# Kernel optimization log

Measured on AMD Instinct MI355X. Metric: run time of the kernel, lower is better.

The kernel has to match this reference:

```python
import jax, jax.numpy as jnp
import numpy as np
import math

N_HEADS = 16
D_MODEL = 1024
HEAD_DIM = D_MODEL // N_HEADS
ROPE_THETA = 10000.0


def _rope_cos_sin(seq_len, head_dim, dtype):
    # freqs = 1/theta^(2i/d), angles = outer(t, freqs)  -> [seq_len, head_dim//2]
    inv_freq = 1.0 / (ROPE_THETA ** (jnp.arange(0, head_dim, 2, dtype=jnp.float32) / head_dim))
    ang = jnp.arange(seq_len, dtype=jnp.float32)[:, None] * inv_freq[None, :]
    return jnp.cos(ang).astype(dtype), jnp.sin(ang).astype(dtype)


def _apply_rope(t, cos, sin):
    # t: [B, N, H, D]; treat last dim as complex pairs (a, b); multiply by e^{i*ang}
    B, N, H, D = t.shape
    tr = t.reshape(B, N, H, D // 2, 2)
    a, b = tr[..., 0], tr[..., 1]
    c = cos[None, :, None, :]  # [1, N, 1, D/2]
    s = sin[None, :, None, :]
    out = jnp.stack([a * c - b * s, a * s + b * c], axis=-1)
    return out.reshape(B, N, H, D)


def setup_inputs() -> dict:
    key = jax.random.key(0)
    ks = jax.random.split(key, 9)
    B, N, D = 4, 2048, D_MODEL
    scale = 0.02
    inp = {"x": jax.random.normal(ks[0], (B, N, D), dtype=jnp.float32)}
    for i, nm in enumerate(["q", "k", "v", "o"]):
        inp[f"w{nm}"] = jax.random.normal(ks[1 + 2 * i], (D, D), dtype=jnp.float32) * scale
        inp[f"b{nm}"] = jax.random.normal(ks[2 + 2 * i], (D,), dtype=jnp.float32) * scale
    return inp


def reference(x, wq, bq, wk, bk, wv, bv, wo, bo):
    B, N, D = x.shape
    H, Hd = N_HEADS, HEAD_DIM
    q = (x @ wq.T + bq).reshape(B, N, H, Hd)
    k = (x @ wk.T + bk).reshape(B, N, H, Hd)
    v = (x @ wv.T + bv).reshape(B, N, H, Hd)
    cos, sin = _rope_cos_sin(N, Hd, x.dtype)
    q = _apply_rope(q, cos, sin)
    k = _apply_rope(k, cos, sin)
    # SDPA, no mask, eval mode (dropout_p = 0)
    scores = jnp.einsum("bqhd,bkhd->bhqk", q, k) / math.sqrt(Hd)
    attn = jax.nn.softmax(scores, axis=-1)
    out = jnp.einsum("bhqk,bkhd->bqhd", attn, v)  # [B, N, H, Hd]
    out = out.reshape(B, N, D)
    return out @ wo.T + bo
```

## Files before the change

### kernel.cpp

```cpp
#include <hip/hip_runtime.h>
#include <math.h>
#include <stdint.h>

#define BBATCH 4
#define NTOK   2048
#define DMOD   1024
#define NH     16
#define HD     64
#define MTOT   8192

typedef __bf16 bf16;
typedef __bf16 bf16x4 __attribute__((ext_vector_type(4)));
typedef __bf16 bf16x8 __attribute__((ext_vector_type(8)));
typedef float  f32x4  __attribute__((ext_vector_type(4)));

typedef __attribute__((address_space(3))) unsigned int lds_u32;
typedef __attribute__((address_space(1))) unsigned int glb_u32;

__device__ __forceinline__ void gload16(const bf16* g, bf16* l) {
    __builtin_amdgcn_global_load_lds((glb_u32*)g, (lds_u32*)l, 16, 0, 0);
}

#define QSCALE 0.1803368801111204f

__global__ void rope_table_kernel(float* __restrict__ ct, float* __restrict__ st) {
    int idx = blockIdx.x * 256 + threadIdx.x;
    if (idx >= NTOK * 32) return;
    int n = idx >> 5, p = idx & 31;
    float inv = powf(10000.0f, -(float)(2 * p) / 64.0f);
    float ang = (float)n * inv;
    ct[idx] = cosf(ang);
    st[idx] = sinf(ang);
}

__global__ __launch_bounds__(256)
void convert_kernel(const float* __restrict__ x,  const float* __restrict__ wq,
                    const float* __restrict__ wk, const float* __restrict__ wv,
                    const float* __restrict__ wo,
                    bf16* __restrict__ xb,  bf16* __restrict__ wqb,
                    bf16* __restrict__ wkb, bf16* __restrict__ wvb,
                    bf16* __restrict__ wob)
{
    const int X4 = (MTOT * DMOD) / 4;
    const int W4 = (DMOD * DMOD) / 4;
    int i = blockIdx.x * 256 + threadIdx.x;
    const float* src; bf16* dst; int off;
    if (i < X4) { src = x; dst = xb; off = i; }
    else {
        int j = i - X4; int w = j / W4; off = j - w * W4;
        src = (w == 0) ? wq : (w == 1) ? wk : (w == 2) ? wv : wo;
        dst = (w == 0) ? wqb : (w == 1) ? wkb : (w == 2) ? wvb : wob;
    }
    float4 v = ((const float4*)src)[off];
    bf16x4 o;
    o[0] = (bf16)v.x; o[1] = (bf16)v.y; o[2] = (bf16)v.z; o[3] = (bf16)v.w;
    *(bf16x4*)(dst + (size_t)off * 4) = o;
}


#define GEMM_PROLOGUE(Aptr, Wptr)                                              \
    __shared__ __align__(16) bf16 As[2][128 * 32];                             \
    __shared__ __align__(16) bf16 Bs[2][128 * 32];                             \
    const int tid = threadIdx.x;                                               \
    const int l   = tid & 63;                                                  \
    const int wid = tid >> 6;                                                  \
    const int wm  = wid >> 1, wn = wid & 1;                                    \
    const int fr  = l & 15, fg = l >> 4;                                       \
    const int srow  = tid >> 2;                                                \
    const int sslot = (tid & 3) ^ ((srow >> 1) & 3);                           \
    const bf16* gA0 = (Aptr) + (size_t)(m0 + srow) * 1024 + sslot * 8;         \
    const bf16* gB0 = (Wptr) + (size_t)(n0 + srow) * 1024 + sslot * 8;         \
    const int aswz = (fg ^ ((fr >> 1) & 3)) * 8;                               \
    int aoff[4], boff[4];                                                      \
    _Pragma("unroll")                                                          \
    for (int i = 0; i < 4; ++i) {                                              \
        aoff[i] = (wm * 64 + i * 16 + fr) * 32 + aswz;                         \
        boff[i] = (wn * 64 + i * 16 + fr) * 32 + aswz;                         \
    }                                                                          \
    f32x4 acc[4][4] = {};

#define GSTAGE(kt, b) do {                                         \
        const bf16* a0_ = gA0 + (kt) * 32;                         \
        const bf16* b0_ = gB0 + (kt) * 32;                         \
        gload16(a0_,                      As[b] + tid * 8);        \
        gload16(a0_ + (size_t)64 * 1024,  As[b] + 2048 + tid * 8); \
        gload16(b0_,                      Bs[b] + tid * 8);        \
        gload16(b0_ + (size_t)64 * 1024,  Bs[b] + 2048 + tid * 8); \
    } while (0)

#define GEMM_KLOOP                                                             \
    GSTAGE(0, 0);                                                              \
    __syncthreads();                                                           \
    int cur = 0;                                                               \
    for (int kt = 0; kt < 32; ++kt) {                                          \
        if (kt < 31) GSTAGE(kt + 1, cur ^ 1);                                  \
        bf16x8 af[4], bfv[4];                                                  \
        _Pragma("unroll")                                                      \
        for (int i = 0; i < 4; ++i) af[i]  = *(const bf16x8*)(As[cur] + aoff[i]); \
        _Pragma("unroll")                                                      \
        for (int i = 0; i < 4; ++i) bfv[i] = *(const bf16x8*)(Bs[cur] + boff[i]); \
        _Pragma("unroll")                                                      \
        for (int mi = 0; mi < 4; ++mi)                                         \
            _Pragma("unroll")                                                  \
            for (int ni = 0; ni < 4; ++ni)                                     \
                acc[mi][ni] = __builtin_amdgcn_mfma_f32_16x16x32_bf16(         \
                    af[mi], bfv[ni], acc[mi][ni], 0, 0, 0);                    \
        __syncthreads();                                                       \
        cur ^= 1;                                                              \
    }

__global__ __launch_bounds__(256)
void gemm_qkv(const bf16* __restrict__ A,
              const bf16* __restrict__ wq, const bf16* __restrict__ wk,
              const bf16* __restrict__ wv,
              const float* __restrict__ bq, const float* __restrict__ bk,
              const float* __restrict__ bv,
              bf16* __restrict__ qb, bf16* __restrict__ kb, bf16* __restrict__ vtb,
              const float* __restrict__ ct, const float* __restrict__ st)
{
    const int sel = blockIdx.x >> 3;
    const int n0  = (blockIdx.x & 7) * 128;
    const int m0  = blockIdx.y * 128;
    const bf16*  W    = (sel == 0) ? wq : (sel == 1) ? wk : wv;
    const float* bias = (sel == 0) ? bq : (sel == 1) ? bk : bv;
    bf16*        out  = (sel == 0) ? qb : (sel == 1) ? kb : vtb;

    GEMM_PROLOGUE(A, W)
    GEMM_KLOOP

    if (sel == 2) {
#pragma unroll
        for (int ni = 0; ni < 4; ++ni) {
            const int col = n0 + wn * 64 + ni * 16 + fr;
            const int h = col >> 6, dd = col & 63;
            const float bvv = bias[col];
#pragma unroll
            for (int mi = 0; mi < 4; ++mi) {
                const int rowb = m0 + wm * 64 + mi * 16 + fg * 4;
                const int bi = rowb >> 11, npb = rowb & (NTOK - 1);
                bf16x4 ov;
#pragma unroll
                for (int r = 0; r < 4; ++r) ov[r] = (bf16)(acc[mi][ni][r] + bvv);
                *(bf16x4*)(out + ((size_t)(bi * NH + h) * HD + dd) * NTOK + npb) = ov;
            }
        }
    } else {
        const float scale = (sel == 0) ? QSCALE : 1.0f;
#pragma unroll
        for (int ni = 0; ni < 4; ++ni) {
            const int col = n0 + wn * 64 + ni * 16 + fr;
            const int h = col >> 6, dd = col & 63, p = (dd >> 1);
            const float bvv = bias[col];
#pragma unroll
            for (int mi = 0; mi < 4; ++mi) {
                const int rowb = m0 + wm * 64 + mi * 16 + fg * 4;
#pragma unroll
                for (int r = 0; r < 4; ++r) {
                    const int row = rowb + r;
                    const int bi = row >> 11, np = row & (NTOK - 1);
                    float v  = acc[mi][ni][r] + bvv;
                    float pv = __shfl_xor(v, 1);
                    float c = ct[np * 32 + p], s = st[np * 32 + p];
                    float o = (dd & 1) ? (pv * s + v * c) : (v * c - pv * s);
                    o *= scale;
                    out[((size_t)(bi * NH + h) * NTOK + np) * HD + dd] = (bf16)o;
                }
            }
        }
    }
}

__global__ __launch_bounds__(256)
void gemm_oproj(const bf16* __restrict__ A, const bf16* __restrict__ W,
                const float* __restrict__ bias, float* __restrict__ out)
{
    const int m0 = blockIdx.y * 128, n0 = blockIdx.x * 128;
    GEMM_PROLOGUE(A, W)
    GEMM_KLOOP
#pragma unroll
    for (int ni = 0; ni < 4; ++ni) {
        const int col = n0 + wn * 64 + ni * 16 + fr;
        const float bv = bias[col];
#pragma unroll
        for (int mi = 0; mi < 4; ++mi) {
            const int rowb = m0 + wm * 64 + mi * 16 + fg * 4;
#pragma unroll
            for (int r = 0; r < 4; ++r)
                out[(size_t)(rowb + r) * 1024 + col] = acc[mi][ni][r] + bv;
        }
    }
}

__global__ __launch_bounds__(256)
void attn_mfma(const bf16* __restrict__ Q, const bf16* __restrict__ K,
               const bf16* __restrict__ Vt, bf16* __restrict__ out)
{
    __shared__ __align__(16) bf16 Ks[2][64 * 64];
    __shared__ __align__(16) bf16 Vs[2][64 * 64];
    __shared__ __align__(16) bf16 Ps[4][32 * 64];

    const int tid = threadIdx.x;
    const int l   = tid & 63;
    const int wid = tid >> 6;
    const int fr  = l & 15, fg = l >> 4;
    const int q0 = blockIdx.x * 128;
    const int bh = blockIdx.y;

    const bf16* Qb = Q  + (size_t)bh * NTOK * HD;
    const bf16* Kb = K  + (size_t)bh * NTOK * HD;
    const bf16* Vb = Vt + (size_t)bh * HD * NTOK;
    bf16* Pw = Ps[wid];

    bf16x8 qf[2][2];
#pragma unroll
    for (int nq = 0; nq < 2; ++nq)
#pragma unroll
        for (int ks = 0; ks < 2; ++ks)
            qf[nq][ks] = *(const bf16x8*)(Qb + (size_t)(q0 + wid * 32 + nq * 16 + fr) * HD
                                          + ks * 32 + fg * 8);

    bf16x8 ones;
#pragma unroll
    for (int i = 0; i < 8; ++i) ones[i] = (bf16)1.0f;

    const int srow  = tid >> 3;
    const int sslot = (tid & 7) ^ (srow & 7);
    const bf16* gK0 = Kb + (size_t)srow * HD + sslot * 8;
    const bf16* gV0 = Vb + (size_t)srow * NTOK + sslot * 8;

#define ASTAGE(t, b) do {                                          \
        const bf16* gK_ = gK0 + (size_t)(t) * 64 * HD;             \
        const bf16* gV_ = gV0 + (size_t)(t) * 64;                  \
        gload16(gK_,                      Ks[b] + tid * 8);        \
        gload16(gK_ + 32 * HD,            Ks[b] + 2048 + tid * 8); \
        gload16(gV_,                      Vs[b] + tid * 8);        \
        gload16(gV_ + (size_t)32 * NTOK,  Vs[b] + 2048 + tid * 8); \
    } while (0)

    f32x4 o[4][2] = {};
    f32x4 l4[2] = {};

    ASTAGE(0, 0);
    __syncthreads();
    int cur = 0;

    for (int t = 0; t < 32; ++t) {
        if (t < 31) ASTAGE(t + 1, cur ^ 1);
        const bf16* Kc = Ks[cur];
        const bf16* Vc = Vs[cur];

        f32x4 tt[4][2] = {};
#pragma unroll
        for (int ks = 0; ks < 2; ++ks) {
            bf16x8 kf[4];
#pragma unroll
            for (int mk = 0; mk < 4; ++mk)
                kf[mk] = *(const bf16x8*)(Kc + (mk * 16 + fr) * 64
                                          + (((ks * 4 + fg) ^ (fr & 7)) * 8));
#pragma unroll
            for (int mk = 0; mk < 4; ++mk)
#pragma unroll
                for (int nq = 0; nq < 2; ++nq)
                    tt[mk][nq] = __builtin_amdgcn_mfma_f32_16x16x32_bf16(
                        kf[mk], qf[nq][ks], tt[mk][nq], 0, 0, 0);
        }

#pragma unroll
        for (int nq = 0; nq < 2; ++nq) {
#pragma unroll
            for (int mk = 0; mk < 4; ++mk) {
                bf16x4 pk;
#pragma unroll
                for (int r = 0; r < 4; ++r)
                    pk[r] = (bf16)__builtin_amdgcn_exp2f(tt[mk][nq][r]);
                *(bf16x4*)(Pw + (nq * 16 + fr) * 64
                           + (((2 * mk + (fg >> 1)) ^ (fr & 7)) * 8) + (fg & 1) * 4) = pk;
            }
        }

#pragma unroll
        for (int ks = 0; ks < 2; ++ks) {
            bf16x8 vf[4], pf[2];
#pragma unroll
            for (int md = 0; md < 4; ++md)
                vf[md] = *(const bf16x8*)(Vc + (md * 16 + fr) * 64
                                          + (((ks * 4 + fg) ^ (fr & 7)) * 8));
#pragma unroll
            for (int nq = 0; nq < 2; ++nq)
                pf[nq] = *(const bf16x8*)(Pw + (nq * 16 + fr) * 64
                                          + (((ks * 4 + fg) ^ (fr & 7)) * 8));
#pragma unroll
            for (int md = 0; md < 4; ++md)
#pragma unroll
                for (int nq = 0; nq < 2; ++nq)
                    o[md][nq] = __builtin_amdgcn_mfma_f32_16x16x32_bf16(
                        vf[md], pf[nq], o[md][nq], 0, 0, 0);
#pragma unroll
            for (int nq = 0; nq < 2; ++nq)
                l4[nq] = __builtin_amdgcn_mfma_f32_16x16x32_bf16(
                    ones, pf[nq], l4[nq], 0, 0, 0);
        }

        __syncthreads();
        cur ^= 1;
    }
#undef ASTAGE

    const int b_ = bh >> 4, h = bh & 15;
#pragma unroll
    for (int nq = 0; nq < 2; ++nq) {
        const float inv = 1.0f / l4[nq][0];
        const int token = q0 + wid * 32 + nq * 16 + fr;
#pragma unroll
        for (int md = 0; md < 4; ++md) {
            bf16x4 ov;
#pragma unroll
            for (int r = 0; r < 4; ++r) ov[r] = (bf16)(o[md][nq][r] * inv);
            *(bf16x4*)(out + (size_t)(b_ * NTOK + token) * DMOD + h * HD + md * 16 + fg * 4) = ov;
        }
    }
}

extern "C" void kernel_launch(void* const* d_in, const int* in_sizes, int n_in,
                              void* d_out, int out_size, void* d_ws, size_t ws_size,
                              hipStream_t stream)
{
    (void)in_sizes; (void)n_in; (void)out_size; (void)ws_size;

    const float* x  = (const float*)d_in[0];
    const float* wq = (const float*)d_in[1];
    const float* bq = (const float*)d_in[2];
    const float* wk = (const float*)d_in[3];
    const float* bk = (const float*)d_in[4];
    const float* wv = (const float*)d_in[5];
    const float* bv = (const float*)d_in[6];
    const float* wo = (const float*)d_in[7];
    const float* bo = (const float*)d_in[8];
    float* out = (float*)d_out;

    const size_t XSZ = (size_t)MTOT * DMOD;
    const size_t WSZ = (size_t)DMOD * DMOD;
    bf16* xb  = (bf16*)d_ws;
    bf16* wqb = xb  + XSZ;
    bf16* wkb = wqb + WSZ;
    bf16* wvb = wkb + WSZ;
    bf16* wob = wvb + WSZ;
    bf16* qb  = wob + WSZ;
    bf16* kb  = qb  + XSZ;
    bf16* vtb = kb  + XSZ;
    bf16* ab  = vtb + XSZ;
    float* ct = (float*)(ab + XSZ);
    float* st = ct + (size_t)NTOK * 32;

    rope_table_kernel<<<dim3(256), dim3(256), 0, stream>>>(ct, st);
    convert_kernel<<<dim3(12288), dim3(256), 0, stream>>>(x, wq, wk, wv, wo,
                                                          xb, wqb, wkb, wvb, wob);

    gemm_qkv<<<dim3(24, MTOT / 128), dim3(256), 0, stream>>>(
        xb, wqb, wkb, wvb, bq, bk, bv, qb, kb, vtb, ct, st);

    attn_mfma<<<dim3(NTOK / 128, BBATCH * NH), dim3(256), 0, stream>>>(qb, kb, vtb, ab);

    gemm_oproj<<<dim3(DMOD / 128, MTOT / 128), dim3(256), 0, stream>>>(ab, wob, bo, out);
}
```

Measured before the change: 324.3 us.

## Switch attention to 32x32 MFMA and keep P in registers via permlane swap

Rewrites the attention inner loop to use 32x32x16 bf16 MFMA tiles instead of 16x16x32. The exponentiated scores are repacked in registers with permlane32_swap so they can feed the PV MFMA directly, which removes the per-wave LDS staging buffer for P and its store/load round trip. The larger tiles also cut K/V fragment LDS reads per MFMA. In exchange the larger accumulators raise register pressure, and correctness depends on the permlane-based layout mapping.

```diff
diff --git a/kernel.cpp b/kernel.cpp
--- a/kernel.cpp
+++ b/kernel.cpp
@@ -10,9 +10,14 @@
 #define MTOT   8192
 
 typedef __bf16 bf16;
+typedef __bf16 bf16x2 __attribute__((ext_vector_type(2)));
 typedef __bf16 bf16x4 __attribute__((ext_vector_type(4)));
 typedef __bf16 bf16x8 __attribute__((ext_vector_type(8)));
 typedef float  f32x4  __attribute__((ext_vector_type(4)));
+typedef float  f32x16 __attribute__((ext_vector_type(16)));
+typedef unsigned int u32;
+typedef unsigned int u32x2 __attribute__((ext_vector_type(2)));
+typedef unsigned int u32x4 __attribute__((ext_vector_type(4)));
 
 typedef __attribute__((address_space(3))) unsigned int lds_u32;
 typedef __attribute__((address_space(1))) unsigned int glb_u32;
@@ -20,6 +25,13 @@
 __device__ __forceinline__ void gload16(const bf16* g, bf16* l) {
     __builtin_amdgcn_global_load_lds((glb_u32*)g, (lds_u32*)l, 16, 0, 0);
 }
+
+__device__ __forceinline__ u32 pack_bf16(float lo, float hi) {
+    bf16x2 z; z[0] = (bf16)lo; z[1] = (bf16)hi;
+    return __builtin_bit_cast(u32, z);
+}
+
+#define MFMA32(a, b, c) __builtin_amdgcn_mfma_f32_32x32x16_bf16((a), (b), (c), 0, 0, 0)
 
 #define QSCALE 0.1803368801111204f
 
@@ -197,27 +209,24 @@
 {
     __shared__ __align__(16) bf16 Ks[2][64 * 64];
     __shared__ __align__(16) bf16 Vs[2][64 * 64];
-    __shared__ __align__(16) bf16 Ps[4][32 * 64];
 
     const int tid = threadIdx.x;
     const int l   = tid & 63;
     const int wid = tid >> 6;
-    const int fr  = l & 15, fg = l >> 4;
+    const int lq  = l & 31;
+    const int hi  = l >> 5;
+    const int rx  = lq & 7;
     const int q0 = blockIdx.x * 128;
     const int bh = blockIdx.y;
 
     const bf16* Qb = Q  + (size_t)bh * NTOK * HD;
     const bf16* Kb = K  + (size_t)bh * NTOK * HD;
     const bf16* Vb = Vt + (size_t)bh * HD * NTOK;
-    bf16* Pw = Ps[wid];
-
-    bf16x8 qf[2][2];
-#pragma unroll
-    for (int nq = 0; nq < 2; ++nq)
-#pragma unroll
-        for (int ks = 0; ks < 2; ++ks)
-            qf[nq][ks] = *(const bf16x8*)(Qb + (size_t)(q0 + wid * 32 + nq * 16 + fr) * HD
-                                          + ks * 32 + fg * 8);
+
+    bf16x8 qf[4];
+#pragma unroll
+    for (int c = 0; c < 4; ++c)
+        qf[c] = *(const bf16x8*)(Qb + (size_t)(q0 + wid * 32 + lq) * HD + c * 16 + hi * 8);
 
     bf16x8 ones;
 #pragma unroll
@@ -237,8 +246,8 @@
         gload16(gV_ + (size_t)32 * NTOK,  Vs[b] + 2048 + tid * 8); \
     } while (0)
 
-    f32x4 o[4][2] = {};
-    f32x4 l4[2] = {};
+    f32x16 o0 = {}, o1 = {};
+    f32x16 l4 = {};
 
     ASTAGE(0, 0);
     __syncthreads();
@@ -249,56 +258,45 @@
         const bf16* Kc = Ks[cur];
         const bf16* Vc = Vs[cur];
 
-        f32x4 tt[4][2] = {};
-#pragma unroll
-        for (int ks = 0; ks < 2; ++ks) {
-            bf16x8 kf[4];
-#pragma unroll
-            for (int mk = 0; mk < 4; ++mk)
-                kf[mk] = *(const bf16x8*)(Kc + (mk * 16 + fr) * 64
-                                          + (((ks * 4 + fg) ^ (fr & 7)) * 8));
-#pragma unroll
-            for (int mk = 0; mk < 4; ++mk)
-#pragma unroll
-                for (int nq = 0; nq < 2; ++nq)
-                    tt[mk][nq] = __builtin_amdgcn_mfma_f32_16x16x32_bf16(
-                        kf[mk], qf[nq][ks], tt[mk][nq], 0, 0, 0);
-        }
-
-#pragma unroll
-        for (int nq = 0; nq < 2; ++nq) {
-#pragma unroll
-            for (int mk = 0; mk < 4; ++mk) {
-                bf16x4 pk;
-#pragma unroll
-                for (int r = 0; r < 4; ++r)
-                    pk[r] = (bf16)__builtin_amdgcn_exp2f(tt[mk][nq][r]);
-                *(bf16x4*)(Pw + (nq * 16 + fr) * 64
-                           + (((2 * mk + (fg >> 1)) ^ (fr & 7)) * 8) + (fg & 1) * 4) = pk;
+        f32x16 t0 = {}, t1 = {};
+#pragma unroll
+        for (int c = 0; c < 4; ++c) {
+            const int slot = ((c * 2 + hi) ^ rx) * 8;
+            bf16x8 kf0 = *(const bf16x8*)(Kc + lq * 64 + slot);
+            bf16x8 kf1 = *(const bf16x8*)(Kc + (32 + lq) * 64 + slot);
+            t0 = MFMA32(kf0, qf[c], t0);
+            t1 = MFMA32(kf1, qf[c], t1);
+        }
+
+#pragma unroll
+        for (int r = 0; r < 16; ++r) t0[r] = __builtin_amdgcn_exp2f(t0[r]);
+#pragma unroll
+        for (int r = 0; r < 16; ++r) t1[r] = __builtin_amdgcn_exp2f(t1[r]);
+
+#pragma unroll
+        for (int b = 0; b < 2; ++b) {
+            const f32x16& tb = b ? t1 : t0;
+#pragma unroll
+            for (int kc = 0; kc < 2; ++kc) {
+                const int a0 = kc ? 8 : 0;
+                const int a1 = kc ? 12 : 4;
+                u32 X  = pack_bf16(tb[a0],     tb[a0 + 1]);
+                u32 Y  = pack_bf16(tb[a1],     tb[a1 + 1]);
+                u32 X2 = pack_bf16(tb[a0 + 2], tb[a0 + 3]);
+                u32 Y2 = pack_bf16(tb[a1 + 2], tb[a1 + 3]);
+                u32x2 s0 = __builtin_amdgcn_permlane32_swap(X,  Y,  false, false);
+                u32x2 s1 = __builtin_amdgcn_permlane32_swap(X2, Y2, false, false);
+                u32x4 bw;
+                bw[0] = s0[0]; bw[1] = s1[0]; bw[2] = s0[1]; bw[3] = s1[1];
+                const bf16x8 pf = __builtin_bit_cast(bf16x8, bw);
+
+                const int slot = (((b * 4 + kc * 2) + hi) ^ rx) * 8;
+                bf16x8 vf0 = *(const bf16x8*)(Vc + lq * 64 + slot);
+                bf16x8 vf1 = *(const bf16x8*)(Vc + (32 + lq) * 64 + slot);
+                o0 = MFMA32(vf0, pf, o0);
+                o1 = MFMA32(vf1, pf, o1);
+                l4 = MFMA32(ones, pf, l4);
             }
-        }
-
-#pragma unroll
-        for (int ks = 0; ks < 2; ++ks) {
-            bf16x8 vf[4], pf[2];
-#pragma unroll
-            for (int md = 0; md < 4; ++md)
-                vf[md] = *(const bf16x8*)(Vc + (md * 16 + fr) * 64
-                                          + (((ks * 4 + fg) ^ (fr & 7)) * 8));
-#pragma unroll
-            for (int nq = 0; nq < 2; ++nq)
-                pf[nq] = *(const bf16x8*)(Pw + (nq * 16 + fr) * 64
-                                          + (((ks * 4 + fg) ^ (fr & 7)) * 8));
-#pragma unroll
-            for (int md = 0; md < 4; ++md)
-#pragma unroll
-                for (int nq = 0; nq < 2; ++nq)
-                    o[md][nq] = __builtin_amdgcn_mfma_f32_16x16x32_bf16(
-                        vf[md], pf[nq], o[md][nq], 0, 0, 0);
-#pragma unroll
-            for (int nq = 0; nq < 2; ++nq)
-                l4[nq] = __builtin_amdgcn_mfma_f32_16x16x32_bf16(
-                    ones, pf[nq], l4[nq], 0, 0, 0);
         }
 
         __syncthreads();
@@ -307,16 +305,18 @@
 #undef ASTAGE
 
     const int b_ = bh >> 4, h = bh & 15;
-#pragma unroll
-    for (int nq = 0; nq < 2; ++nq) {
-        const float inv = 1.0f / l4[nq][0];
-        const int token = q0 + wid * 32 + nq * 16 + fr;
-#pragma unroll
-        for (int md = 0; md < 4; ++md) {
+    const float inv = 1.0f / l4[0];
+    const int token = q0 + wid * 32 + lq;
+    bf16* dst = out + (size_t)(b_ * NTOK + token) * DMOD + h * HD;
+#pragma unroll
+    for (int dblk = 0; dblk < 2; ++dblk) {
+        const f32x16& ob = dblk ? o1 : o0;
+#pragma unroll
+        for (int g = 0; g < 4; ++g) {
             bf16x4 ov;
 #pragma unroll
-            for (int r = 0; r < 4; ++r) ov[r] = (bf16)(o[md][nq][r] * inv);
-            *(bf16x4*)(out + (size_t)(b_ * NTOK + token) * DMOD + h * HD + md * 16 + fg * 4) = ov;
+            for (int r2 = 0; r2 < 4; ++r2) ov[r2] = (bf16)(ob[g * 4 + r2] * inv);
+            *(bf16x4*)(dst + dblk * 32 + g * 8 + hi * 4) = ov;
         }
     }
 }
```

Measured after the change: 325.9 us. About the same (+0.5%).
